# Kernel optimization log

Hardware: AMD Instinct MI355X
Metric: run time of the kernel (lower is better)

The kernel has to match this reference:

```python
import jax, jax.numpy as jnp
import numpy as np

B, L, E = 2, 2048, 1024
H = 16
DH = E // H  # head dim for qk and v (dim_qk=dim_v=embed_dim)
HID = 4 * E  # fcn_dim_factor * dim_v
SCALE = DH ** 0.5


def setup_inputs() -> dict:
    key = jax.random.key(0)
    ks = jax.random.split(key, 12)
    s = lambda fan_in: 1.0 / np.sqrt(fan_in)
    return {
        "x": jax.random.uniform(ks[0], (B, L), jnp.float32),
        "z": jax.random.normal(ks[1], (B, L, E), jnp.float32),
        "Wq": jax.random.normal(ks[2], (E, E), jnp.float32) * s(E),
        "bq": jnp.zeros((E,), jnp.float32),
        "Wk": jax.random.normal(ks[3], (E, E), jnp.float32) * s(E),
        "bk": jnp.zeros((E,), jnp.float32),
        "Wv": jax.random.normal(ks[4], (E, E), jnp.float32) * s(E),
        "bv": jnp.zeros((E,), jnp.float32),
        "W1": jax.random.normal(ks[5], (E, HID), jnp.float32) * s(E),
        "b1": jnp.zeros((HID,), jnp.float32),
        "W2": jax.random.normal(ks[6], (HID, 1), jnp.float32) * s(HID),
        "b2": jnp.zeros((1,), jnp.float32),
    }


def reference(x, z, Wq, bq, Wk, bk, Wv, bv, W1, b1, W2, b2):
    # Projections -> (B, H, L, DH)
    def heads(t):
        return t.reshape(B, L, H, DH).transpose(0, 2, 1, 3)

    Q = heads(z @ Wq + bq)
    K = heads(z @ Wk + bk)
    V = heads(z @ Wv + bv)

    # Scores (B, H, L, L)
    S = jnp.einsum("bhid,bhjd->bhij", Q, K) / SCALE

    # Weighted softmax along query axis (dim=-2), weighted by population x
    w = x[:, None, :, None]  # (B, 1, L, 1), broadcasts over queries i
    m = jnp.max(S, axis=-2, keepdims=True)
    e = w * jnp.exp(S - m)
    A = e / jnp.sum(e, axis=-2, keepdims=True)

    # V scaled by population weight, then AV
    V_scaled = w * V
    O = jnp.einsum("bhij,bhjd->bhid", A, V_scaled)  # (B, H, L, DH)
    O = O.transpose(0, 2, 1, 3).reshape(B, L, H * DH)

    # FFN: Linear -> GELU (exact) -> Linear(->1) -> squeeze
    y = jax.nn.gelu(O @ W1 + b1, approximate=False)
    y = (y @ W2 + b2).squeeze(-1)  # (B, L)
    return y
```

## Files before the change

### kernel.cpp

```cpp
#include <hip/hip_runtime.h>
#include <hip/hip_bf16.h>
#include <math.h>

#define B_    2
#define L_    2048
#define E_    1024
#define H_    16
#define DH_   64
#define HID_  4096
#define NROW_ (B_*L_)
#define BH_   (B_*H_)

#define QSCL  0.18033688011112042f

typedef __attribute__((ext_vector_type(8)))  short    short8v;
typedef _Float16 half8v __attribute__((ext_vector_type(8)));
typedef __attribute__((ext_vector_type(16))) float    f32x16;

#define MFMA32(A, Bv, C) __builtin_amdgcn_mfma_f32_32x32x16_bf16((A), (Bv), (C), 0, 0, 0)
#define MFMAH(A, Bv, C)  __builtin_amdgcn_mfma_f32_32x32x16_f16((A), (Bv), (C), 0, 0, 0)

#define WAITV(N) asm volatile("s_waitcnt vmcnt(" #N ")" ::: "memory")
#define SBAR()   __builtin_amdgcn_s_barrier()

__device__ __forceinline__ unsigned short f2bf(float f) {
    union { float f; unsigned u; } v; v.f = f;
    return (unsigned short)((v.u + 0x8000u) >> 16);
}
__device__ __forceinline__ unsigned pack2_bf16(float lo, float hi) {
    union { float f; unsigned u; } a, b; a.f = lo; b.f = hi;
    return __builtin_amdgcn_perm(b.u + 0x8000u, a.u + 0x8000u, 0x07060302u);
}
__device__ __forceinline__ float bf2f(unsigned short u) {
    union { unsigned u; float f; } v; v.u = ((unsigned)u) << 16;
    return v.f;
}

__device__ __forceinline__ void gl_lds16(const void* g, void* l) {
    __builtin_amdgcn_global_load_lds(
        (const __attribute__((address_space(1))) unsigned int*)g,
        (__attribute__((address_space(3))) unsigned int*)l, 16, 0, 0);
}

__device__ __forceinline__ float erf_fast(float v) {
    float a = fabsf(v);
    float t = __builtin_amdgcn_rcpf(1.0f + 0.3275911f * a);
    float p = t * (0.254829592f + t * (-0.284496736f + t * (1.421413741f +
              t * (-1.453152027f + t * 1.061405429f))));
    float r = 1.0f - p * __expf(-a * a);
    return copysignf(r, v);
}

__global__ __launch_bounds__(256) void zh_prep(
    const float* __restrict__ z, _Float16* __restrict__ zh)
{
    const size_t i = ((size_t)blockIdx.x * 256 + threadIdx.x) * 8;
    float4 a = *(const float4*)&z[i];
    float4 b = *(const float4*)&z[i + 4];
    union { _Float16 h[8]; half8v v; } o;
    o.h[0] = (_Float16)a.x; o.h[1] = (_Float16)a.y;
    o.h[2] = (_Float16)a.z; o.h[3] = (_Float16)a.w;
    o.h[4] = (_Float16)b.x; o.h[5] = (_Float16)b.y;
    o.h[6] = (_Float16)b.z; o.h[7] = (_Float16)b.w;
    *(half8v*)&zh[i] = o.v;
}

__global__ __launch_bounds__(256) void wprep3(
    const float* __restrict__ Wq, const float* __restrict__ Wk,
    const float* __restrict__ Wv,
    _Float16* __restrict__ Tq, _Float16* __restrict__ Tk,
    _Float16* __restrict__ Tv)
{
    const float* src = (blockIdx.z == 0) ? Wq : (blockIdx.z == 1) ? Wk : Wv;
    _Float16*    dst = (blockIdx.z == 0) ? Tq : (blockIdx.z == 1) ? Tk : Tv;
    __shared__ float tile[64][65];
    const int t  = threadIdx.x;
    const int r0 = blockIdx.y * 64, c0 = blockIdx.x * 64;
    #pragma unroll
    for (int u = 0; u < 4; ++u) {
        int f = t + 256 * u, row = f >> 4, c4 = (f & 15) << 2;
        *(float4*)&tile[row][c4] = *(const float4*)&src[(size_t)(r0 + row) * E_ + c0 + c4];
    }
    __syncthreads();
    #pragma unroll
    for (int u = 0; u < 4; ++u) {
        int f = t + 256 * u, c = f >> 4, r4 = (f & 15) << 2;
        union { _Float16 h[4]; uint2 u2; } pk;
        pk.h[0] = (_Float16)tile[r4 + 0][c];
        pk.h[1] = (_Float16)tile[r4 + 1][c];
        pk.h[2] = (_Float16)tile[r4 + 2][c];
        pk.h[3] = (_Float16)tile[r4 + 3][c];
        *(uint2*)&dst[(size_t)(c0 + c) * E_ + r0 + r4] = pk.u2;
    }
}

__global__ __launch_bounds__(256) void w1prep(
    const float* __restrict__ W1, _Float16* __restrict__ W1t)
{
    __shared__ float tile[64][65];
    const int t  = threadIdx.x;
    const int r0 = blockIdx.y * 64, c0 = blockIdx.x * 64;
    #pragma unroll
    for (int u = 0; u < 4; ++u) {
        int f = t + 256 * u, row = f >> 4, c4 = (f & 15) << 2;
        *(float4*)&tile[row][c4] = *(const float4*)&W1[(size_t)(r0 + row) * HID_ + c0 + c4];
    }
    __syncthreads();
    #pragma unroll
    for (int u = 0; u < 4; ++u) {
        int f = t + 256 * u, c = f >> 4, r4 = (f & 15) << 2;
        union { _Float16 h[4]; uint2 u2; } pk;
        pk.h[0] = (_Float16)tile[r4 + 0][c];
        pk.h[1] = (_Float16)tile[r4 + 1][c];
        pk.h[2] = (_Float16)tile[r4 + 2][c];
        pk.h[3] = (_Float16)tile[r4 + 3][c];
        *(uint2*)&W1t[(size_t)(c0 + c) * E_ + r0 + r4] = pk.u2;
    }
}

__global__ __launch_bounds__(256) void qkv_mfma(
    const _Float16* __restrict__ zh,
    const _Float16* __restrict__ Tall,
    const float* __restrict__ bq, const float* __restrict__ bk,
    const float* __restrict__ bv,
    unsigned short* __restrict__ outQKV)
{
    const int which = blockIdx.y >> 3;
    const float* bias = (which == 0) ? bq : (which == 1) ? bk : bv;
    const float  osc  = (which == 0) ? QSCL : 1.0f;
    unsigned short* out = outQKV + (size_t)which * ((size_t)BH_ * L_ * DH_);

    __shared__ _Float16 Ah[2][128 * 64];
    __shared__ _Float16 Bs[2][128 * 64];

    const int t    = threadIdx.x;
    const int lane = t & 63;
    const int w    = t >> 6;
    const int l31  = lane & 31;
    const int hq   = lane >> 5;
    const int wm   = w >> 1, wn = w & 1;
    const int m0   = blockIdx.x * 128;
    const int n0   = blockIdx.y * 128;

    const int srow0 = (lane >> 3);
    const int ssl   = lane & 7;

    f32x16 acc[2][2] = {};

#define QKV_STAGE(bb, kc)                                                          \
    {                                                                              \
        _Pragma("unroll")                                                          \
        for (int u = 0; u < 4; ++u) {                                              \
            int ch  = w * 4 + u;                                                   \
            int row = ch * 8 + srow0;                                              \
            gl_lds16(&zh[(size_t)(m0 + row) * E_ + (kc) * 64 + ((ssl ^ (row & 7)) << 3)], \
                     &Ah[bb][ch * 512]);                                           \
            gl_lds16(&Tall[(size_t)(n0 + row) * E_ + (kc) * 64 + ((ssl ^ (row & 7)) << 3)], \
                     &Bs[bb][ch * 512]);                                           \
        }                                                                          \
    }

    QKV_STAGE(0, 0);
    QKV_STAGE(1, 1);
    __syncthreads();
    int cur = 0;

    for (int kc = 0; kc < 16; ++kc) {
        if (kc < 15) WAITV(8); else WAITV(0);
        SBAR();
        __builtin_amdgcn_s_setprio(1);
        #pragma unroll
        for (int ks = 0; ks < 4; ++ks) {
            half8v fb[2];
            #pragma unroll
            for (int nb = 0; nb < 2; ++nb) {
                int br = wn * 64 + nb * 32 + l31;
                fb[nb] = *(const half8v*)&Bs[cur][br * 64 + (((ks * 2 + hq) ^ (br & 7)) << 3)];
            }
            #pragma unroll
            for (int mb = 0; mb < 2; ++mb) {
                int ar = wm * 64 + mb * 32 + l31;
                half8v fa = *(const half8v*)&Ah[cur][ar * 64 + (((ks * 2 + hq) ^ (ar & 7)) << 3)];
                acc[mb][0] = MFMAH(fa, fb[0], acc[mb][0]);
                acc[mb][1] = MFMAH(fa, fb[1], acc[mb][1]);
            }
        }
        __builtin_amdgcn_s_setprio(0);
        SBAR();
        if (kc + 2 < 16) QKV_STAGE(cur, kc + 2);
        cur ^= 1;
    }

    #pragma unroll
    for (int nb = 0; nb < 2; ++nb) {
        int n  = n0 + wn * 64 + nb * 32 + l31;
        int nn = n & 1023;
        int h  = nn >> 6, dh = nn & 63;
        float bb = bias[nn];
        #pragma unroll
        for (int mb = 0; mb < 2; ++mb) {
            #pragma unroll
            for (int r = 0; r < 16; ++r) {
                int m  = m0 + wm * 64 + mb * 32 + (r & 3) + 8 * (r >> 2) + 4 * hq;
                int b  = m >> 11, i = m & (L_ - 1);
                out[((size_t)(b * H_ + h) * L_ + i) * DH_ + dh] = f2bf((acc[mb][nb][r] + bb) * osc);
            }
        }
    }
#undef QKV_STAGE
}

__global__ __launch_bounds__(256) void col_stats_mfma(
    const unsigned short* __restrict__ Qb, const unsigned short* __restrict__ Kb,
    const float* __restrict__ x, float* __restrict__ Do)
{
    __shared__ unsigned short Qlds[2][128 * 64];
    __shared__ float xlds[L_];

    const int t    = threadIdx.x;
    const int lane = t & 63;
    const int wv   = t >> 6;
    const int l31  = lane & 31;
    const int hq   = lane >> 5;
    const int bh   = blockIdx.y;
    const int b    = bh >> 4;
    const int j0   = blockIdx.x * 256 + wv * 64;

    const int srow0 = (lane >> 3);
    const int ssl   = lane & 7;

    #pragma unroll
    for (int u = 0; u < 2; ++u) {
        int f = t + 256 * u;
        *(float4*)&xlds[f * 4] = *(const float4*)&x[(size_t)b * L_ + f * 4];
    }

    short8v kf[2][4];
    #pragma unroll
    for (int s = 0; s < 2; ++s) {
        const unsigned short* kp = Kb + ((size_t)bh * L_ + j0 + s * 32 + l31) * DH_ + hq * 8;
        #pragma unroll
        for (int c = 0; c < 4; ++c) kf[s][c] = *(const short8v*)(kp + c * 16);
    }

    float d0[16], d1[16];
    #pragma unroll
    for (int r = 0; r < 16; ++r) { d0[r] = 0.f; d1[r] = 0.f; }

#define CS_STAGE(bb, ich)                                                           \
    {                                                                               \
        _Pragma("unroll")                                                           \
        for (int u = 0; u < 4; ++u) {                                               \
            int ch  = wv * 4 + u;                                                   \
            int row = ch * 8 + srow0;                                               \
            gl_lds16(&Qb[((size_t)bh * L_ + (ich) * 128 + row) * DH_ + ((ssl ^ (row & 7)) << 3)], \
                     &Qlds[bb][ch * 512]);                                          \
        }                                                                           \
    }

    CS_STAGE(0, 0);
    CS_STAGE(1, 1);
    __syncthreads();
    int cur = 0;

    const int NT = L_ / 128;
    for (int ich = 0; ich < NT; ++ich) {
        if (ich < NT - 1) WAITV(4); else WAITV(0);
        SBAR();
        #pragma unroll
        for (int cc = 0; cc < 4; ++cc) {
            f32x16 a0 = {}, a1 = {};
            __builtin_amdgcn_s_setprio(1);
            #pragma unroll
            for (int c = 0; c < 4; ++c) {
                int qr = cc * 32 + l31;
                short8v qv = *(const short8v*)&Qlds[cur][qr * 64 + (((c * 2 + hq) ^ (qr & 7)) << 3)];
                a0 = MFMA32(kf[0][c], qv, a0);
                a1 = MFMA32(kf[1][c], qv, a1);
            }
            __builtin_amdgcn_s_setprio(0);
            float xi = xlds[ich * 128 + cc * 32 + l31];
            #pragma unroll
            for (int r = 0; r < 16; ++r) {
                d0[r] += xi * __builtin_amdgcn_exp2f(a0[r]);
                d1[r] += xi * __builtin_amdgcn_exp2f(a1[r]);
            }
        }
        SBAR();
        if (ich + 2 < NT) CS_STAGE(cur, ich + 2);
        cur ^= 1;
    }

    #pragma unroll
    for (int r = 0; r < 16; ++r) {
        #pragma unroll
        for (int off = 16; off > 0; off >>= 1) {
            d0[r] += __shfl_xor(d0[r], off);
            d1[r] += __shfl_xor(d1[r], off);
        }
    }
    if (l31 == 0) {
        #pragma unroll
        for (int r = 0; r < 16; ++r) {
            int jr = 4 * hq + (r & 3) + 8 * (r >> 2);
            Do[(size_t)bh * L_ + j0 + jr]      = d0[r];
            Do[(size_t)bh * L_ + j0 + 32 + jr] = d1[r];
        }
    }
#undef CS_STAGE
}

__global__ __launch_bounds__(256) void vt_prep(
    const unsigned short* __restrict__ Vb, const float* __restrict__ x,
    const float* __restrict__ Do, unsigned short* __restrict__ Vt)
{
    const int bh = blockIdx.y;
    const int b  = bh >> 4;
    const int j  = blockIdx.x * 256 + threadIdx.x;
    const float s = x[(size_t)b * L_ + j] / Do[(size_t)bh * L_ + j];
    const unsigned short* vp = Vb + ((size_t)bh * L_ + j) * DH_;
    #pragma unroll
    for (int c = 0; c < 16; ++c) {
        ushort4 v = *(const ushort4*)&vp[c * 4];
        Vt[((size_t)bh * DH_ + c * 4 + 0) * L_ + j] = f2bf(bf2f(v.x) * s);
        Vt[((size_t)bh * DH_ + c * 4 + 1) * L_ + j] = f2bf(bf2f(v.y) * s);
        Vt[((size_t)bh * DH_ + c * 4 + 2) * L_ + j] = f2bf(bf2f(v.z) * s);
        Vt[((size_t)bh * DH_ + c * 4 + 3) * L_ + j] = f2bf(bf2f(v.w) * s);
    }
}

__global__ __launch_bounds__(256) void attn_out_mfma(
    const unsigned short* __restrict__ Qb, const unsigned short* __restrict__ Kb,
    const unsigned short* __restrict__ Vt, const float* __restrict__ x,
    _Float16* __restrict__ Of)
{
    __shared__ unsigned short Klds[2][64 * 64];
    __shared__ unsigned short Vlds[2][64 * 64];

    const int t    = threadIdx.x;
    const int lane = t & 63;
    const int wv   = t >> 6;
    const int l31  = lane & 31;
    const int hq   = lane >> 5;
    const int bh   = blockIdx.y;
    const int b    = bh >> 4, hh = bh & 15;
    const int iw   = blockIdx.x * 256 + wv * 64;

    const int srow0 = (lane >> 3);
    const int ssl   = lane & 7;

    short8v qf[2][4];
    #pragma unroll
    for (int ig = 0; ig < 2; ++ig) {
        const unsigned short* qp = Qb + ((size_t)bh * L_ + iw + ig * 32 + l31) * DH_ + hq * 8;
        #pragma unroll
        for (int c = 0; c < 4; ++c) qf[ig][c] = *(const short8v*)(qp + c * 16);
    }

    f32x16 accO[2][2] = {};

#define AO_STAGE(bb, jt)                                                            \
    {                                                                               \
        _Pragma("unroll")                                                           \
        for (int u = 0; u < 2; ++u) {                                               \
            int ch  = wv * 2 + u;                                                   \
            int row = ch * 8 + srow0;                                               \
            gl_lds16(&Kb[((size_t)bh * L_ + (jt) * 64 + row) * DH_ + ((ssl ^ (row & 7)) << 3)], \
                     &Klds[bb][ch * 512]);                                          \
            gl_lds16(&Vt[((size_t)bh * DH_ + row) * L_ + (jt) * 64 + ((ssl ^ (row & 7)) << 3)], \
                     &Vlds[bb][ch * 512]);                                          \
        }                                                                           \
    }

    AO_STAGE(0, 0);
    AO_STAGE(1, 1);
    __syncthreads();
    int cur = 0;

    const int NT = L_ / 64;
    for (int jt = 0; jt < NT; ++jt) {
        if (jt < NT - 1) WAITV(4); else WAITV(0);
        SBAR();

        uint4 pa[2][4];
        #pragma unroll
        for (int js = 0; js < 2; ++js) {
            f32x16 as0 = {}, as1 = {};
            __builtin_amdgcn_s_setprio(1);
            #pragma unroll
            for (int c = 0; c < 4; ++c) {
                int krow = js * 32 + l31;
                short8v kfr = *(const short8v*)&Klds[cur][krow * 64 + (((c * 2 + hq) ^ (krow & 7)) << 3)];
                as0 = MFMA32(kfr, qf[0][c], as0);
                as1 = MFMA32(kfr, qf[1][c], as1);
            }
            __builtin_amdgcn_s_setprio(0);
            #pragma unroll
            for (int ig = 0; ig < 2; ++ig) {
                const f32x16& as = (ig == 0) ? as0 : as1;
                float p[16];
                #pragma unroll
                for (int r = 0; r < 16; ++r) p[r] = __builtin_amdgcn_exp2f(as[r]);

                unsigned P0 = pack2_bf16(p[0], p[1]);
                unsigned P1 = pack2_bf16(p[2], p[3]);
                unsigned Q0 = pack2_bf16(p[4], p[5]);
                unsigned Q1 = pack2_bf16(p[6], p[7]);
                asm("v_permlane32_swap_b32 %0, %1" : "+v"(P0), "+v"(Q0));
                asm("v_permlane32_swap_b32 %0, %1" : "+v"(P1), "+v"(Q1));
                pa[ig][js * 2 + 0] = make_uint4(P0, P1, Q0, Q1);

                unsigned R0 = pack2_bf16(p[8],  p[9]);
                unsigned R1 = pack2_bf16(p[10], p[11]);
                unsigned S0 = pack2_bf16(p[12], p[13]);
                unsigned S1 = pack2_bf16(p[14], p[15]);
                asm("v_permlane32_swap_b32 %0, %1" : "+v"(R0), "+v"(S0));
                asm("v_permlane32_swap_b32 %0, %1" : "+v"(R1), "+v"(S1));
                pa[ig][js * 2 + 1] = make_uint4(R0, R1, S0, S1);
            }
        }

        __builtin_amdgcn_s_setprio(1);
        #pragma unroll
        for (int c = 0; c < 4; ++c) {
            union { uint4 u; short8v s; } pa0, pa1;
            pa0.u = pa[0][c]; pa1.u = pa[1][c];
            int r0 = l31, r1 = 32 + l31;
            short8v vf0 = *(const short8v*)&Vlds[cur][r0 * 64 + (((c * 2 + hq) ^ (r0 & 7)) << 3)];
            short8v vf1 = *(const short8v*)&Vlds[cur][r1 * 64 + (((c * 2 + hq) ^ (r1 & 7)) << 3)];
            accO[0][0] = MFMA32(pa0.s, vf0, accO[0][0]);
            accO[0][1] = MFMA32(pa0.s, vf1, accO[0][1]);
            accO[1][0] = MFMA32(pa1.s, vf0, accO[1][0]);
            accO[1][1] = MFMA32(pa1.s, vf1, accO[1][1]);
        }
        __builtin_amdgcn_s_setprio(0);
        SBAR();
        if (jt + 2 < NT) AO_STAGE(cur, jt + 2);
        cur ^= 1;
    }

    #pragma unroll
    for (int ig = 0; ig < 2; ++ig) {
        #pragma unroll
        for (int q = 0; q < 4; ++q) {
            float4 xq = *(const float4*)&x[(size_t)b * L_ + iw + ig * 32 + 4 * hq + 8 * q];
            const float xs[4] = { xq.x, xq.y, xq.z, xq.w };
            #pragma unroll
            for (int k = 0; k < 4; ++k) {
                int r    = q * 4 + k;
                int irow = iw + ig * 32 + 4 * hq + 8 * q + k;
                size_t base = ((size_t)b * L_ + irow) * E_ + hh * DH_;
                Of[base + l31]      = (_Float16)(accO[ig][0][r] * xs[k]);
                Of[base + 32 + l31] = (_Float16)(accO[ig][1][r] * xs[k]);
            }
        }
    }
#undef AO_STAGE
}

__global__ __launch_bounds__(256) void y_init(float* __restrict__ y, const float* __restrict__ b2)
{
    y[blockIdx.x * 256 + threadIdx.x] = b2[0];
}

__global__ __launch_bounds__(256) void mlp_mfma(
    const _Float16* __restrict__ Of, const _Float16* __restrict__ W1t,
    const float* __restrict__ b1, const float* __restrict__ W2,
    float* __restrict__ y)
{
    __shared__ _Float16 Oh[2][128 * 64];
    __shared__ _Float16 Wh[2][128 * 64];

    const int t    = threadIdx.x;
    const int lane = t & 63;
    const int w    = t >> 6;
    const int l31  = lane & 31;
    const int hq   = lane >> 5;
    const int wm   = w >> 1, wn = w & 1;
    const int m0   = blockIdx.x * 128;
    const int n0   = blockIdx.y * 128;

    const int srow0 = (lane >> 3);
    const int ssl   = lane & 7;

    f32x16 acc[2][2] = {};

#define MLP_STAGE(bb, kc)                                                          \
    {                                                                              \
        _Pragma("unroll")                                                          \
        for (int u = 0; u < 4; ++u) {                                              \
            int ch  = w * 4 + u;                                                   \
            int row = ch * 8 + srow0;                                              \
            gl_lds16(&Of[(size_t)(m0 + row) * E_ + (kc) * 64 + ((ssl ^ (row & 7)) << 3)], \
                     &Oh[bb][ch * 512]);                                           \
            gl_lds16(&W1t[(size_t)(n0 + row) * E_ + (kc) * 64 + ((ssl ^ (row & 7)) << 3)], \
                     &Wh[bb][ch * 512]);                                           \
        }                                                                          \
    }

    MLP_STAGE(0, 0);
    MLP_STAGE(1, 1);
    __syncthreads();
    int cur = 0;

    for (int kc = 0; kc < 16; ++kc) {
        if (kc < 15) WAITV(8); else WAITV(0);
        SBAR();
        __builtin_amdgcn_s_setprio(1);
        #pragma unroll
        for (int ks = 0; ks < 4; ++ks) {
            half8v fb[2];
            #pragma unroll
            for (int nb = 0; nb < 2; ++nb) {
                int br = wn * 64 + nb * 32 + l31;
                fb[nb] = *(const half8v*)&Wh[cur][br * 64 + (((ks * 2 + hq) ^ (br & 7)) << 3)];
            }
            #pragma unroll
            for (int mb = 0; mb < 2; ++mb) {
                int ar = wm * 64 + mb * 32 + l31;
                half8v fa = *(const half8v*)&Oh[cur][ar * 64 + (((ks * 2 + hq) ^ (ar & 7)) << 3)];
                acc[mb][0] = MFMAH(fa, fb[0], acc[mb][0]);
                acc[mb][1] = MFMAH(fa, fb[1], acc[mb][1]);
            }
        }
        __builtin_amdgcn_s_setprio(0);
        SBAR();
        if (kc + 2 < 16) MLP_STAGE(cur, kc + 2);
        cur ^= 1;
    }

    const int hid0 = n0 + wn * 64 + l31;
    const float bb0 = b1[hid0],      w20 = W2[hid0];
    const float bb1 = b1[hid0 + 32], w21 = W2[hid0 + 32];
    #pragma unroll
    for (int mb = 0; mb < 2; ++mb) {
        #pragma unroll
        for (int r = 0; r < 16; ++r) {
            float h0 = acc[mb][0][r] + bb0;
            float h1 = acc[mb][1][r] + bb1;
            float s  = 0.5f * h0 * (1.0f + erf_fast(h0 * 0.70710678f)) * w20
                     + 0.5f * h1 * (1.0f + erf_fast(h1 * 0.70710678f)) * w21;
            #pragma unroll
            for (int off = 16; off > 0; off >>= 1) s += __shfl_xor(s, off);
            if (l31 == 0) {
                int m = m0 + wm * 64 + mb * 32 + (r & 3) + 8 * (r >> 2) + 4 * hq;
                atomicAdd(&y[m], s);
            }
        }
    }
#undef MLP_STAGE
}

extern "C" void kernel_launch(void* const* d_in, const int* in_sizes, int n_in,
                              void* d_out, int out_size, void* d_ws, size_t ws_size,
                              hipStream_t stream)
{
    const float* x  = (const float*)d_in[0];
    const float* z  = (const float*)d_in[1];
    const float* Wq = (const float*)d_in[2];
    const float* bq = (const float*)d_in[3];
    const float* Wk = (const float*)d_in[4];
    const float* bk = (const float*)d_in[5];
    const float* Wv = (const float*)d_in[6];
    const float* bv = (const float*)d_in[7];
    const float* W1 = (const float*)d_in[8];
    const float* b1 = (const float*)d_in[9];
    const float* W2 = (const float*)d_in[10];
    const float* b2 = (const float*)d_in[11];
    float* y = (float*)d_out;

    const size_t NQ = (size_t)BH_ * L_ * DH_;
    unsigned short* p = (unsigned short*)d_ws;
    unsigned short* Qb  = p;  p += NQ;
    unsigned short* Kb  = p;  p += NQ;
    unsigned short* Vb  = p;  p += NQ;
    unsigned short* Vt  = p;  p += NQ;
    _Float16* zh  = (_Float16*)p;  p += (size_t)NROW_ * E_;
    _Float16* Tq  = (_Float16*)p;  p += (size_t)E_ * E_;
    _Float16* Tk  = (_Float16*)p;  p += (size_t)E_ * E_;
    _Float16* Tv  = (_Float16*)p;  p += (size_t)E_ * E_;
    _Float16* W1t = (_Float16*)p;  p += (size_t)HID_ * E_;
    _Float16* Ofp = (_Float16*)p;  p += (size_t)NROW_ * E_;
    float* Dw = (float*)p;

    zh_prep<<<dim3((NROW_ * E_) / (256 * 8)), 256, 0, stream>>>(z, zh);
    wprep3 <<<dim3(E_ / 64, E_ / 64, 3), 256, 0, stream>>>(Wq, Wk, Wv, Tq, Tk, Tv);
    w1prep <<<dim3(HID_ / 64, E_ / 64), 256, 0, stream>>>(W1, W1t);

    qkv_mfma<<<dim3(NROW_ / 128, 3 * E_ / 128), 256, 0, stream>>>(
        zh, Tq, bq, bk, bv, Qb);

    col_stats_mfma<<<dim3(L_ / 256, BH_), 256, 0, stream>>>(Qb, Kb, x, Dw);

    vt_prep<<<dim3(L_ / 256, BH_), 256, 0, stream>>>(Vb, x, Dw, Vt);

    attn_out_mfma<<<dim3(L_ / 256, BH_), 256, 0, stream>>>(Qb, Kb, Vt, x, Ofp);

    y_init<<<dim3(NROW_ / 256), 256, 0, stream>>>(y, b2);

    mlp_mfma<<<dim3(NROW_ / 128, HID_ / 128), 256, 0, stream>>>(
        Ofp, W1t, b1, W2, y);
}
```

Before: 217.4 us.

## Split attention key range across two wave groups and reduce via LDS

The attention output kernel now launches 512 threads per block, and two groups of four waves each process half of the key range for the same 256 queries. Each group keeps its own double-buffered K/V tiles in LDS. The partial accumulators are combined through a shared-memory buffer before the final scaled store. The goal is to raise waves per CU and latency hiding for a grid of only 256 blocks. The cost is more LDS (about 100KB per block) and an extra reduction step.

```diff
diff --git a/kernel.cpp b/kernel.cpp
--- a/kernel.cpp
+++ b/kernel.cpp
@@ -329,22 +329,25 @@
     }
 }
 
-__global__ __launch_bounds__(256) void attn_out_mfma(
+__global__ __launch_bounds__(512) void attn_out_mfma(
     const unsigned short* __restrict__ Qb, const unsigned short* __restrict__ Kb,
     const unsigned short* __restrict__ Vt, const float* __restrict__ x,
     _Float16* __restrict__ Of)
 {
-    __shared__ unsigned short Klds[2][64 * 64];
-    __shared__ unsigned short Vlds[2][64 * 64];
+    __shared__ unsigned short Klds[2][2][64 * 64];
+    __shared__ unsigned short Vlds[2][2][64 * 64];
+    __shared__ float comb[4][64 * 67];
 
     const int t    = threadIdx.x;
     const int lane = t & 63;
     const int wv   = t >> 6;
+    const int iwv  = wv & 3;
+    const int jh   = wv >> 2;
     const int l31  = lane & 31;
     const int hq   = lane >> 5;
     const int bh   = blockIdx.y;
     const int b    = bh >> 4, hh = bh & 15;
-    const int iw   = blockIdx.x * 256 + wv * 64;
+    const int iw   = blockIdx.x * 256 + iwv * 64;
 
     const int srow0 = (lane >> 3);
     const int ssl   = lane & 7;
@@ -363,23 +366,22 @@
     {                                                                               \
         _Pragma("unroll")                                                           \
         for (int u = 0; u < 2; ++u) {                                               \
-            int ch  = wv * 2 + u;                                                   \
+            int ch  = iwv * 2 + u;                                                  \
             int row = ch * 8 + srow0;                                               \
             gl_lds16(&Kb[((size_t)bh * L_ + (jt) * 64 + row) * DH_ + ((ssl ^ (row & 7)) << 3)], \
-                     &Klds[bb][ch * 512]);                                          \
+                     &Klds[jh][bb][ch * 512]);                                      \
             gl_lds16(&Vt[((size_t)bh * DH_ + row) * L_ + (jt) * 64 + ((ssl ^ (row & 7)) << 3)], \
-                     &Vlds[bb][ch * 512]);                                          \
+                     &Vlds[jh][bb][ch * 512]);                                      \
         }                                                                           \
     }
 
-    AO_STAGE(0, 0);
-    AO_STAGE(1, 1);
+    AO_STAGE(0, jh * 16 + 0);
+    AO_STAGE(1, jh * 16 + 1);
     __syncthreads();
     int cur = 0;
 
-    const int NT = L_ / 64;
-    for (int jt = 0; jt < NT; ++jt) {
-        if (jt < NT - 1) WAITV(4); else WAITV(0);
+    for (int ltj = 0; ltj < 16; ++ltj) {
+        if (ltj < 15) WAITV(4); else WAITV(0);
         SBAR();
 
         uint4 pa[2][4];
@@ -390,7 +392,7 @@
             #pragma unroll
             for (int c = 0; c < 4; ++c) {
                 int krow = js * 32 + l31;
-                short8v kfr = *(const short8v*)&Klds[cur][krow * 64 + (((c * 2 + hq) ^ (krow & 7)) << 3)];
+                short8v kfr = *(const short8v*)&Klds[jh][cur][krow * 64 + (((c * 2 + hq) ^ (krow & 7)) << 3)];
                 as0 = MFMA32(kfr, qf[0][c], as0);
                 as1 = MFMA32(kfr, qf[1][c], as1);
             }
@@ -426,8 +428,8 @@
             union { uint4 u; short8v s; } pa0, pa1;
             pa0.u = pa[0][c]; pa1.u = pa[1][c];
             int r0 = l31, r1 = 32 + l31;
-            short8v vf0 = *(const short8v*)&Vlds[cur][r0 * 64 + (((c * 2 + hq) ^ (r0 & 7)) << 3)];
-            short8v vf1 = *(const short8v*)&Vlds[cur][r1 * 64 + (((c * 2 + hq) ^ (r1 & 7)) << 3)];
+            short8v vf0 = *(const short8v*)&Vlds[jh][cur][r0 * 64 + (((c * 2 + hq) ^ (r0 & 7)) << 3)];
+            short8v vf1 = *(const short8v*)&Vlds[jh][cur][r1 * 64 + (((c * 2 + hq) ^ (r1 & 7)) << 3)];
             accO[0][0] = MFMA32(pa0.s, vf0, accO[0][0]);
             accO[0][1] = MFMA32(pa0.s, vf1, accO[0][1]);
             accO[1][0] = MFMA32(pa1.s, vf0, accO[1][0]);
@@ -435,23 +437,45 @@
         }
         __builtin_amdgcn_s_setprio(0);
         SBAR();
-        if (jt + 2 < NT) AO_STAGE(cur, jt + 2);
+        if (ltj + 2 < 16) AO_STAGE(cur, jh * 16 + ltj + 2);
         cur ^= 1;
     }
 
-    #pragma unroll
-    for (int ig = 0; ig < 2; ++ig) {
-        #pragma unroll
-        for (int q = 0; q < 4; ++q) {
-            float4 xq = *(const float4*)&x[(size_t)b * L_ + iw + ig * 32 + 4 * hq + 8 * q];
-            const float xs[4] = { xq.x, xq.y, xq.z, xq.w };
-            #pragma unroll
-            for (int k = 0; k < 4; ++k) {
-                int r    = q * 4 + k;
-                int irow = iw + ig * 32 + 4 * hq + 8 * q + k;
-                size_t base = ((size_t)b * L_ + irow) * E_ + hh * DH_;
-                Of[base + l31]      = (_Float16)(accO[ig][0][r] * xs[k]);
-                Of[base + 32 + l31] = (_Float16)(accO[ig][1][r] * xs[k]);
+    if (jh == 1) {
+        float* cb = &comb[iwv][lane * 67];
+        #pragma unroll
+        for (int g = 0; g < 2; ++g)
+            #pragma unroll
+            for (int h = 0; h < 2; ++h)
+                #pragma unroll
+                for (int r = 0; r < 16; ++r)
+                    cb[(g * 2 + h) * 16 + r] = accO[g][h][r];
+    }
+    __syncthreads();
+    if (jh == 0) {
+        const float* cb = &comb[iwv][lane * 67];
+        #pragma unroll
+        for (int g = 0; g < 2; ++g)
+            #pragma unroll
+            for (int h = 0; h < 2; ++h)
+                #pragma unroll
+                for (int r = 0; r < 16; ++r)
+                    accO[g][h][r] += cb[(g * 2 + h) * 16 + r];
+
+        #pragma unroll
+        for (int ig = 0; ig < 2; ++ig) {
+            #pragma unroll
+            for (int q = 0; q < 4; ++q) {
+                float4 xq = *(const float4*)&x[(size_t)b * L_ + iw + ig * 32 + 4 * hq + 8 * q];
+                const float xs[4] = { xq.x, xq.y, xq.z, xq.w };
+                #pragma unroll
+                for (int k = 0; k < 4; ++k) {
+                    int r    = q * 4 + k;
+                    int irow = iw + ig * 32 + 4 * hq + 8 * q + k;
+                    size_t base = ((size_t)b * L_ + irow) * E_ + hh * DH_;
+                    Of[base + l31]      = (_Float16)(accO[ig][0][r] * xs[k]);
+                    Of[base + 32 + l31] = (_Float16)(accO[ig][1][r] * xs[k]);
+                }
             }
         }
     }
@@ -594,7 +618,7 @@
 
     vt_prep<<<dim3(L_ / 256, BH_), 256, 0, stream>>>(Vb, x, Dw, Vt);
 
-    attn_out_mfma<<<dim3(L_ / 256, BH_), 256, 0, stream>>>(Qb, Kb, Vt, x, Ofp);
+    attn_out_mfma<<<dim3(L_ / 256, BH_), 512, 0, stream>>>(Qb, Kb, Vt, x, Ofp);
 
     y_init<<<dim3(NROW_ / 256), 256, 0, stream>>>(y, b2);
 
```

Result: faster. 207.1 us (-4.7%).
